# Kernel optimization log

Hardware: AMD Instinct MI355X
Metric: run time of the kernel (lower is better)

## Reference

```python
import jax, jax.numpy as jnp
import numpy as np

N = 50000
E = 800000
IN_DIM = 128
OUT_DIM = 128


def setup_inputs() -> dict:
    key = jax.random.key(0)
    k1, k2, k3, k4 = jax.random.split(key, 4)
    x = jax.random.normal(k1, (N, IN_DIM), dtype=jnp.float32)
    edge_index = jax.random.randint(k2, (2, E), 0, N, dtype=jnp.int64)
    # Linear(in_dim*2, out_dim) params
    W = jax.random.normal(k3, (2 * IN_DIM, OUT_DIM), dtype=jnp.float32) * (1.0 / np.sqrt(2 * IN_DIM))
    b = jax.random.normal(k4, (OUT_DIM,), dtype=jnp.float32) * 0.01
    return {"x": x, "edge_index": edge_index, "W": W, "b": b}


def reference(x, edge_index, W, b):
    src, dst = edge_index[0], edge_index[1]
    diff = x[src] - x[dst]                              # (E, C)
    # segment-max over destination nodes; empty segments get -inf identity
    seg_max = jax.ops.segment_max(diff, dst, num_segments=N)  # (N, C)
    counts = jax.ops.segment_sum(jnp.ones((E,), dtype=jnp.int32), dst, num_segments=N)
    # original code leaves zeros for nodes with no incoming edges
    max_diff = jnp.where((counts > 0)[:, None], seg_max, jnp.zeros_like(seg_max))
    x_cat = jnp.concatenate([x, max_diff], axis=-1)     # (N, 2C)
    return x_cat @ W + b
```

## Files before the change

### kernel.cpp

```cpp
#include <hip/hip_runtime.h>
#include <math.h>

#define NN 50000
#define NE 800000
#define CD 128
#define PB 3200
#define OVCAP 65536

typedef __attribute__((ext_vector_type(8))) short short8;
typedef __attribute__((ext_vector_type(4))) float f32x4;
typedef unsigned long long ull;


__device__ inline unsigned pack2bf(float lo, float hi) {
    unsigned a = __float_as_uint(lo), b = __float_as_uint(hi);
    a = (a + 0x7fffu + ((a >> 16) & 1u)) >> 16;
    b = (b + 0x7fffu + ((b >> 16) & 1u)) & 0xffff0000u;
    return a | b;
}

__device__ inline unsigned short f2bf(float f) {
    unsigned u = __float_as_uint(f);
    return (unsigned short)((u + 0x7fffu + ((u >> 16) & 1u)) >> 16);
}

__device__ inline void fmax8(float* m, uint4 v) {
    m[0] = fmaxf(m[0], __uint_as_float(v.x << 16));
    m[1] = fmaxf(m[1], __uint_as_float(v.x & 0xffff0000u));
    m[2] = fmaxf(m[2], __uint_as_float(v.y << 16));
    m[3] = fmaxf(m[3], __uint_as_float(v.y & 0xffff0000u));
    m[4] = fmaxf(m[4], __uint_as_float(v.z << 16));
    m[5] = fmaxf(m[5], __uint_as_float(v.z & 0xffff0000u));
    m[6] = fmaxf(m[6], __uint_as_float(v.w << 16));
    m[7] = fmaxf(m[7], __uint_as_float(v.w & 0xffff0000u));
}


__global__ __launch_bounds__(256) void prep_k(const int* __restrict__ ei,
                                              const float* __restrict__ x,
                                              const float* __restrict__ W,
                                              int* __restrict__ cnt,
                                              unsigned short* __restrict__ bkt,
                                              unsigned* __restrict__ ovl,
                                              unsigned* __restrict__ xb,
                                              unsigned short* __restrict__ wt) {
    int tid0 = blockIdx.x * 256 + threadIdx.x;
    int phase = blockIdx.x & 1;

    for (int p = 0; p < 2; p++) {
        if ((p ^ phase) == 0) {
            for (int e = tid0; e < NE; e += PB * 256) {
                int s = ei[e];
                int d = ei[NE + e];
                int k = atomicAdd(&cnt[d], 1);
                if (k < 64) {
                    bkt[(size_t)d * 64 + k] = (unsigned short)s;
                } else {
                    unsigned oi = atomicAdd((unsigned*)&cnt[NN], 1u);
                    if (oi < OVCAP) ovl[oi] = ((unsigned)d << 16) | (unsigned)s;
                }
            }
        } else {
            for (int i = tid0; i < NN * CD / 4; i += PB * 256) {
                float4 v = ((const float4*)x)[i];
                uint2 r;
                r.x = pack2bf(v.x, v.y);
                r.y = pack2bf(v.z, v.w);
                ((uint2*)xb)[i] = r;
            }
        }
    }
    for (int i = tid0; i < 2 * CD * CD; i += PB * 256) {
        int n = i >> 8, k = i & 255;
        wt[(size_t)n * 256 + k] = f2bf(W[(size_t)k * 128 + n]);
    }
}


__global__ __launch_bounds__(256) void fused_k(const unsigned* __restrict__ xb,
                                               const int* __restrict__ cnt,
                                               const unsigned short* __restrict__ bkt,
                                               const unsigned* __restrict__ ovl,
                                               const short* __restrict__ wt,
                                               const float* __restrict__ bias,
                                               float* __restrict__ out) {
    __shared__ unsigned short amx[32][136];

    int t = threadIdx.x;
    int nbase = blockIdx.x * 32;
    int w = t >> 6, lane = t & 63;
    int q = lane >> 4, c = lane & 15;

#pragma unroll 1
    for (int j = 0; j < 2; j++) {
        int ln = w * 8 + j * 4 + q;
        int node = nbase + ln;
        int cntv = (node < NN) ? cnt[node] : 0;
        int cn = min(cntv, 64);
        const unsigned short* brow = bkt + (size_t)node * 64;
        float m[8];
#pragma unroll
        for (int i = 0; i < 8; i++) m[i] = -INFINITY;

        for (int base = 0; base < cn; base += 8) {
            uint4 pk = *(const uint4*)(brow + base);
            int s0 = (int)(pk.x & 0xffffu), s1 = (int)(pk.x >> 16);
            int s2 = (int)(pk.y & 0xffffu), s3 = (int)(pk.y >> 16);
            int s4 = (int)(pk.z & 0xffffu), s5 = (int)(pk.z >> 16);
            int s6 = (int)(pk.w & 0xffffu), s7 = (int)(pk.w >> 16);
            if (base + 8 <= cn) {
                fmax8(m, *(const uint4*)(xb + (size_t)s0 * 64 + c * 4));
                fmax8(m, *(const uint4*)(xb + (size_t)s1 * 64 + c * 4));
                fmax8(m, *(const uint4*)(xb + (size_t)s2 * 64 + c * 4));
                fmax8(m, *(const uint4*)(xb + (size_t)s3 * 64 + c * 4));
                fmax8(m, *(const uint4*)(xb + (size_t)s4 * 64 + c * 4));
                fmax8(m, *(const uint4*)(xb + (size_t)s5 * 64 + c * 4));
                fmax8(m, *(const uint4*)(xb + (size_t)s6 * 64 + c * 4));
                fmax8(m, *(const uint4*)(xb + (size_t)s7 * 64 + c * 4));
            } else {
                if (base + 0 < cn) fmax8(m, *(const uint4*)(xb + (size_t)s0 * 64 + c * 4));
                if (base + 1 < cn) fmax8(m, *(const uint4*)(xb + (size_t)s1 * 64 + c * 4));
                if (base + 2 < cn) fmax8(m, *(const uint4*)(xb + (size_t)s2 * 64 + c * 4));
                if (base + 3 < cn) fmax8(m, *(const uint4*)(xb + (size_t)s3 * 64 + c * 4));
                if (base + 4 < cn) fmax8(m, *(const uint4*)(xb + (size_t)s4 * 64 + c * 4));
                if (base + 5 < cn) fmax8(m, *(const uint4*)(xb + (size_t)s5 * 64 + c * 4));
                if (base + 6 < cn) fmax8(m, *(const uint4*)(xb + (size_t)s6 * 64 + c * 4));
                if (base + 7 < cn) fmax8(m, *(const uint4*)(xb + (size_t)s7 * 64 + c * 4));
            }
        }
        if (cntv > 64) {
            unsigned no = (unsigned)cnt[NN];
            if (no > OVCAP) no = OVCAP;
            for (unsigned i2 = 0; i2 < no; i2++) {
                unsigned u = ovl[i2];
                if ((int)(u >> 16) == node)
                    fmax8(m, *(const uint4*)(xb + (size_t)(u & 0xffffu) * 64 + c * 4));
            }
        }
        uint4 r = make_uint4(0u, 0u, 0u, 0u);
        if (cntv > 0) {
            uint4 xd = *(const uint4*)(xb + (size_t)node * 64 + c * 4);
            float d0 = m[0] - __uint_as_float(xd.x << 16);
            float d1 = m[1] - __uint_as_float(xd.x & 0xffff0000u);
            float d2 = m[2] - __uint_as_float(xd.y << 16);
            float d3 = m[3] - __uint_as_float(xd.y & 0xffff0000u);
            float d4 = m[4] - __uint_as_float(xd.z << 16);
            float d5 = m[5] - __uint_as_float(xd.z & 0xffff0000u);
            float d6 = m[6] - __uint_as_float(xd.w << 16);
            float d7 = m[7] - __uint_as_float(xd.w & 0xffff0000u);
            r.x = pack2bf(d0, d1);
            r.y = pack2bf(d2, d3);
            r.z = pack2bf(d4, d5);
            r.w = pack2bf(d6, d7);
        }
        *(uint4*)&amx[ln][c * 8] = r;
    }
    __syncthreads();

    int mm = lane & 15, g = lane >> 4;
    int rt = w & 1, ch = w >> 1;
    int r0 = nbase + rt * 16;
    int row = r0 + mm;
    bool rowok = row < NN;

    f32x4 acc[4];
#pragma unroll
    for (int ct = 0; ct < 4; ct++) {
        float bv = bias[ch * 64 + ct * 16 + mm];
        acc[ct] = (f32x4){bv, bv, bv, bv};
    }

    const short* xbs = (const short*)xb;
#pragma unroll
    for (int kc = 0; kc < 8; kc++) {
        int k0 = kc * 32;
        short8 a;
        if (kc < 4) {
            a = (short8){0, 0, 0, 0, 0, 0, 0, 0};
            if (rowok) a = *(const short8*)(xbs + (size_t)row * 128 + k0 + g * 8);
        } else {
            a = *(const short8*)&amx[rt * 16 + mm][(k0 - 128) + g * 8];
        }
#pragma unroll
        for (int ct = 0; ct < 4; ct++) {
            short8 b = *(const short8*)(wt + (size_t)(ch * 64 + ct * 16 + mm) * 256 + k0 + g * 8);
            acc[ct] = __builtin_amdgcn_mfma_f32_16x16x32_bf16(a, b, acc[ct], 0, 0, 0);
        }
    }

#pragma unroll
    for (int ct = 0; ct < 4; ct++) {
#pragma unroll
        for (int i = 0; i < 4; i++) {
            int rr = r0 + g * 4 + i;
            if (rr < NN) out[(size_t)rr * 128 + ch * 64 + ct * 16 + mm] = acc[ct][i];
        }
    }
}


extern "C" void kernel_launch(void* const* d_in, const int* in_sizes, int n_in,
                              void* d_out, int out_size, void* d_ws, size_t ws_size,
                              hipStream_t stream) {
    const float* x = (const float*)d_in[0];
    const int* ei = (const int*)d_in[1];
    const float* W = (const float*)d_in[2];
    const float* bias = (const float*)d_in[3];
    float* out = (float*)d_out;

    int* wsi = (int*)d_ws;
    int* cnt = wsi;
    unsigned short* bkt = (unsigned short*)(wsi + 50016);
    unsigned* xb = (unsigned*)(wsi + 1650016);
    unsigned short* wt = (unsigned short*)(wsi + 4850016);
    unsigned* ovl = (unsigned*)(wsi + 4866400);

    hipMemsetAsync(cnt, 0, 50016 * sizeof(int), stream);

    prep_k<<<PB, 256, 0, stream>>>(ei, x, W, cnt, bkt, ovl, xb, wt);
    fused_k<<<(NN + 31) / 32, 256, 0, stream>>>(xb, cnt, bkt, ovl, (const short*)wt,
                                                bias, out);
}
```

Baseline: 190.8 us.

## Merge prep and fused kernels into one cooperative persistent kernel with grid sync

Combines the bucketing/conversion kernel and the gather-max-plus-MFMA kernel into a single cooperative launch, separated by a grid-wide barrier. The second phase becomes a persistent loop over node tiles. The aim is to remove one kernel launch and the gap between the two kernels. In exchange the grid size is capped by occupancy, the prep phase has fewer threads, a grid sync is added, and the cooperative launch has its own overhead.

```diff
diff --git a/kernel.cpp b/kernel.cpp
--- a/kernel.cpp
+++ b/kernel.cpp
@@ -1,10 +1,13 @@
 #include <hip/hip_runtime.h>
+#include <hip/hip_cooperative_groups.h>
 #include <math.h>
+
+namespace cg = cooperative_groups;
 
 #define NN 50000
 #define NE 800000
 #define CD 128
-#define PB 3200
+#define NTILE 1563
 #define OVCAP 65536
 
 typedef __attribute__((ext_vector_type(8))) short short8;
@@ -36,20 +39,26 @@
 }
 
 
-__global__ __launch_bounds__(256) void prep_k(const int* __restrict__ ei,
-                                              const float* __restrict__ x,
-                                              const float* __restrict__ W,
-                                              int* __restrict__ cnt,
-                                              unsigned short* __restrict__ bkt,
-                                              unsigned* __restrict__ ovl,
-                                              unsigned* __restrict__ xb,
-                                              unsigned short* __restrict__ wt) {
-    int tid0 = blockIdx.x * 256 + threadIdx.x;
+__global__ __launch_bounds__(256, 4) void mono_k(const int* __restrict__ ei,
+                                                 const float* __restrict__ x,
+                                                 const float* __restrict__ W,
+                                                 const float* __restrict__ bias,
+                                                 float* __restrict__ out,
+                                                 int* __restrict__ cnt,
+                                                 unsigned short* __restrict__ bkt,
+                                                 unsigned* __restrict__ ovl,
+                                                 unsigned* __restrict__ xb,
+                                                 unsigned short* __restrict__ wt) {
+    __shared__ unsigned short amx[32][136];
+
+    int t = threadIdx.x;
+    int tid0 = blockIdx.x * 256 + t;
+    int gsz = gridDim.x * 256;
     int phase = blockIdx.x & 1;
 
     for (int p = 0; p < 2; p++) {
         if ((p ^ phase) == 0) {
-            for (int e = tid0; e < NE; e += PB * 256) {
+            for (int e = tid0; e < NE; e += gsz) {
                 int s = ei[e];
                 int d = ei[NE + e];
                 int k = atomicAdd(&cnt[d], 1);
@@ -61,7 +70,7 @@
                 }
             }
         } else {
-            for (int i = tid0; i < NN * CD / 4; i += PB * 256) {
+            for (int i = tid0; i < NN * CD / 4; i += gsz) {
                 float4 v = ((const float4*)x)[i];
                 uint2 r;
                 r.x = pack2bf(v.x, v.y);
@@ -70,131 +79,125 @@
             }
         }
     }
-    for (int i = tid0; i < 2 * CD * CD; i += PB * 256) {
+    for (int i = tid0; i < 2 * CD * CD; i += gsz) {
         int n = i >> 8, k = i & 255;
         wt[(size_t)n * 256 + k] = f2bf(W[(size_t)k * 128 + n]);
     }
-}
-
-
-__global__ __launch_bounds__(256) void fused_k(const unsigned* __restrict__ xb,
-                                               const int* __restrict__ cnt,
-                                               const unsigned short* __restrict__ bkt,
-                                               const unsigned* __restrict__ ovl,
-                                               const short* __restrict__ wt,
-                                               const float* __restrict__ bias,
-                                               float* __restrict__ out) {
-    __shared__ unsigned short amx[32][136];
-
-    int t = threadIdx.x;
-    int nbase = blockIdx.x * 32;
+
+    cg::this_grid().sync();
+
     int w = t >> 6, lane = t & 63;
     int q = lane >> 4, c = lane & 15;
-
-#pragma unroll 1
-    for (int j = 0; j < 2; j++) {
-        int ln = w * 8 + j * 4 + q;
-        int node = nbase + ln;
-        int cntv = (node < NN) ? cnt[node] : 0;
-        int cn = min(cntv, 64);
-        const unsigned short* brow = bkt + (size_t)node * 64;
-        float m[8];
-#pragma unroll
-        for (int i = 0; i < 8; i++) m[i] = -INFINITY;
-
-        for (int base = 0; base < cn; base += 8) {
-            uint4 pk = *(const uint4*)(brow + base);
-            int s0 = (int)(pk.x & 0xffffu), s1 = (int)(pk.x >> 16);
-            int s2 = (int)(pk.y & 0xffffu), s3 = (int)(pk.y >> 16);
-            int s4 = (int)(pk.z & 0xffffu), s5 = (int)(pk.z >> 16);
-            int s6 = (int)(pk.w & 0xffffu), s7 = (int)(pk.w >> 16);
-            if (base + 8 <= cn) {
-                fmax8(m, *(const uint4*)(xb + (size_t)s0 * 64 + c * 4));
-                fmax8(m, *(const uint4*)(xb + (size_t)s1 * 64 + c * 4));
-                fmax8(m, *(const uint4*)(xb + (size_t)s2 * 64 + c * 4));
-                fmax8(m, *(const uint4*)(xb + (size_t)s3 * 64 + c * 4));
-                fmax8(m, *(const uint4*)(xb + (size_t)s4 * 64 + c * 4));
-                fmax8(m, *(const uint4*)(xb + (size_t)s5 * 64 + c * 4));
-                fmax8(m, *(const uint4*)(xb + (size_t)s6 * 64 + c * 4));
-                fmax8(m, *(const uint4*)(xb + (size_t)s7 * 64 + c * 4));
-            } else {
-                if (base + 0 < cn) fmax8(m, *(const uint4*)(xb + (size_t)s0 * 64 + c * 4));
-                if (base + 1 < cn) fmax8(m, *(const uint4*)(xb + (size_t)s1 * 64 + c * 4));
-                if (base + 2 < cn) fmax8(m, *(const uint4*)(xb + (size_t)s2 * 64 + c * 4));
-                if (base + 3 < cn) fmax8(m, *(const uint4*)(xb + (size_t)s3 * 64 + c * 4));
-                if (base + 4 < cn) fmax8(m, *(const uint4*)(xb + (size_t)s4 * 64 + c * 4));
-                if (base + 5 < cn) fmax8(m, *(const uint4*)(xb + (size_t)s5 * 64 + c * 4));
-                if (base + 6 < cn) fmax8(m, *(const uint4*)(xb + (size_t)s6 * 64 + c * 4));
-                if (base + 7 < cn) fmax8(m, *(const uint4*)(xb + (size_t)s7 * 64 + c * 4));
-            }
-        }
-        if (cntv > 64) {
-            unsigned no = (unsigned)cnt[NN];
-            if (no > OVCAP) no = OVCAP;
-            for (unsigned i2 = 0; i2 < no; i2++) {
-                unsigned u = ovl[i2];
-                if ((int)(u >> 16) == node)
-                    fmax8(m, *(const uint4*)(xb + (size_t)(u & 0xffffu) * 64 + c * 4));
-            }
-        }
-        uint4 r = make_uint4(0u, 0u, 0u, 0u);
-        if (cntv > 0) {
-            uint4 xd = *(const uint4*)(xb + (size_t)node * 64 + c * 4);
-            float d0 = m[0] - __uint_as_float(xd.x << 16);
-            float d1 = m[1] - __uint_as_float(xd.x & 0xffff0000u);
-            float d2 = m[2] - __uint_as_float(xd.y << 16);
-            float d3 = m[3] - __uint_as_float(xd.y & 0xffff0000u);
-            float d4 = m[4] - __uint_as_float(xd.z << 16);
-            float d5 = m[5] - __uint_as_float(xd.z & 0xffff0000u);
-            float d6 = m[6] - __uint_as_float(xd.w << 16);
-            float d7 = m[7] - __uint_as_float(xd.w & 0xffff0000u);
-            r.x = pack2bf(d0, d1);
-            r.y = pack2bf(d2, d3);
-            r.z = pack2bf(d4, d5);
-            r.w = pack2bf(d6, d7);
-        }
-        *(uint4*)&amx[ln][c * 8] = r;
-    }
-    __syncthreads();
-
     int mm = lane & 15, g = lane >> 4;
     int rt = w & 1, ch = w >> 1;
-    int r0 = nbase + rt * 16;
-    int row = r0 + mm;
-    bool rowok = row < NN;
-
-    f32x4 acc[4];
-#pragma unroll
-    for (int ct = 0; ct < 4; ct++) {
-        float bv = bias[ch * 64 + ct * 16 + mm];
-        acc[ct] = (f32x4){bv, bv, bv, bv};
-    }
-
-    const short* xbs = (const short*)xb;
-#pragma unroll
-    for (int kc = 0; kc < 8; kc++) {
-        int k0 = kc * 32;
-        short8 a;
-        if (kc < 4) {
-            a = (short8){0, 0, 0, 0, 0, 0, 0, 0};
-            if (rowok) a = *(const short8*)(xbs + (size_t)row * 128 + k0 + g * 8);
-        } else {
-            a = *(const short8*)&amx[rt * 16 + mm][(k0 - 128) + g * 8];
-        }
+
+    for (int tile = blockIdx.x; tile < NTILE; tile += gridDim.x) {
+        int nbase = tile * 32;
+
+#pragma unroll 1
+        for (int j = 0; j < 2; j++) {
+            int ln = w * 8 + j * 4 + q;
+            int node = nbase + ln;
+            int cntv = (node < NN) ? cnt[node] : 0;
+            int cn = min(cntv, 64);
+            const unsigned short* brow = bkt + (size_t)node * 64;
+            float m[8];
+#pragma unroll
+            for (int i = 0; i < 8; i++) m[i] = -INFINITY;
+
+            for (int base = 0; base < cn; base += 8) {
+                uint4 pk = *(const uint4*)(brow + base);
+                int s0 = (int)(pk.x & 0xffffu), s1 = (int)(pk.x >> 16);
+                int s2 = (int)(pk.y & 0xffffu), s3 = (int)(pk.y >> 16);
+                int s4 = (int)(pk.z & 0xffffu), s5 = (int)(pk.z >> 16);
+                int s6 = (int)(pk.w & 0xffffu), s7 = (int)(pk.w >> 16);
+                if (base + 8 <= cn) {
+                    fmax8(m, *(const uint4*)(xb + (size_t)s0 * 64 + c * 4));
+                    fmax8(m, *(const uint4*)(xb + (size_t)s1 * 64 + c * 4));
+                    fmax8(m, *(const uint4*)(xb + (size_t)s2 * 64 + c * 4));
+                    fmax8(m, *(const uint4*)(xb + (size_t)s3 * 64 + c * 4));
+                    fmax8(m, *(const uint4*)(xb + (size_t)s4 * 64 + c * 4));
+                    fmax8(m, *(const uint4*)(xb + (size_t)s5 * 64 + c * 4));
+                    fmax8(m, *(const uint4*)(xb + (size_t)s6 * 64 + c * 4));
+                    fmax8(m, *(const uint4*)(xb + (size_t)s7 * 64 + c * 4));
+                } else {
+                    if (base + 0 < cn) fmax8(m, *(const uint4*)(xb + (size_t)s0 * 64 + c * 4));
+                    if (base + 1 < cn) fmax8(m, *(const uint4*)(xb + (size_t)s1 * 64 + c * 4));
+                    if (base + 2 < cn) fmax8(m, *(const uint4*)(xb + (size_t)s2 * 64 + c * 4));
+                    if (base + 3 < cn) fmax8(m, *(const uint4*)(xb + (size_t)s3 * 64 + c * 4));
+                    if (base + 4 < cn) fmax8(m, *(const uint4*)(xb + (size_t)s4 * 64 + c * 4));
+                    if (base + 5 < cn) fmax8(m, *(const uint4*)(xb + (size_t)s5 * 64 + c * 4));
+                    if (base + 6 < cn) fmax8(m, *(const uint4*)(xb + (size_t)s6 * 64 + c * 4));
+                    if (base + 7 < cn) fmax8(m, *(const uint4*)(xb + (size_t)s7 * 64 + c * 4));
+                }
+            }
+            if (cntv > 64) {
+                unsigned no = (unsigned)cnt[NN];
+                if (no > OVCAP) no = OVCAP;
+                for (unsigned i2 = 0; i2 < no; i2++) {
+                    unsigned u = ovl[i2];
+                    if ((int)(u >> 16) == node)
+                        fmax8(m, *(const uint4*)(xb + (size_t)(u & 0xffffu) * 64 + c * 4));
+                }
+            }
+            uint4 r = make_uint4(0u, 0u, 0u, 0u);
+            if (cntv > 0) {
+                uint4 xd = *(const uint4*)(xb + (size_t)node * 64 + c * 4);
+                float d0 = m[0] - __uint_as_float(xd.x << 16);
+                float d1 = m[1] - __uint_as_float(xd.x & 0xffff0000u);
+                float d2 = m[2] - __uint_as_float(xd.y << 16);
+                float d3 = m[3] - __uint_as_float(xd.y & 0xffff0000u);
+                float d4 = m[4] - __uint_as_float(xd.z << 16);
+                float d5 = m[5] - __uint_as_float(xd.z & 0xffff0000u);
+                float d6 = m[6] - __uint_as_float(xd.w << 16);
+                float d7 = m[7] - __uint_as_float(xd.w & 0xffff0000u);
+                r.x = pack2bf(d0, d1);
+                r.y = pack2bf(d2, d3);
+                r.z = pack2bf(d4, d5);
+                r.w = pack2bf(d6, d7);
+            }
+            *(uint4*)&amx[ln][c * 8] = r;
+        }
+        __syncthreads();
+
+        int r0 = nbase + rt * 16;
+        int row = r0 + mm;
+        bool rowok = row < NN;
+
+        f32x4 acc[4];
 #pragma unroll
         for (int ct = 0; ct < 4; ct++) {
-            short8 b = *(const short8*)(wt + (size_t)(ch * 64 + ct * 16 + mm) * 256 + k0 + g * 8);
-            acc[ct] = __builtin_amdgcn_mfma_f32_16x16x32_bf16(a, b, acc[ct], 0, 0, 0);
-        }
-    }
-
-#pragma unroll
-    for (int ct = 0; ct < 4; ct++) {
-#pragma unroll
-        for (int i = 0; i < 4; i++) {
-            int rr = r0 + g * 4 + i;
-            if (rr < NN) out[(size_t)rr * 128 + ch * 64 + ct * 16 + mm] = acc[ct][i];
-        }
+            float bv = bias[ch * 64 + ct * 16 + mm];
+            acc[ct] = (f32x4){bv, bv, bv, bv};
+        }
+
+        const short* xbs = (const short*)xb;
+#pragma unroll
+        for (int kc = 0; kc < 8; kc++) {
+            int k0 = kc * 32;
+            short8 a;
+            if (kc < 4) {
+                a = (short8){0, 0, 0, 0, 0, 0, 0, 0};
+                if (rowok) a = *(const short8*)(xbs + (size_t)row * 128 + k0 + g * 8);
+            } else {
+                a = *(const short8*)&amx[rt * 16 + mm][(k0 - 128) + g * 8];
+            }
+#pragma unroll
+            for (int ct = 0; ct < 4; ct++) {
+                short8 b = *(const short8*)(wt + (size_t)(ch * 64 + ct * 16 + mm) * 256 + k0 + g * 8);
+                acc[ct] = __builtin_amdgcn_mfma_f32_16x16x32_bf16(a, b, acc[ct], 0, 0, 0);
+            }
+        }
+
+#pragma unroll
+        for (int ct = 0; ct < 4; ct++) {
+#pragma unroll
+            for (int i = 0; i < 4; i++) {
+                int rr = r0 + g * 4 + i;
+                if (rr < NN) out[(size_t)rr * 128 + ch * 64 + ct * 16 + mm] = acc[ct][i];
+            }
+        }
+        __syncthreads();
     }
 }
 
@@ -215,9 +218,20 @@
     unsigned short* wt = (unsigned short*)(wsi + 4850016);
     unsigned* ovl = (unsigned*)(wsi + 4866400);
 
+    static int gridBlocks = 0;
+    if (gridBlocks == 0) {
+        int perCU = 0, numCU = 0;
+        hipOccupancyMaxActiveBlocksPerMultiprocessor(&perCU, (const void*)mono_k, 256, 0);
+        hipDeviceGetAttribute(&numCU, hipDeviceAttributeMultiprocessorCount, 0);
+        long gb = (long)perCU * (long)numCU;
+        if (gb < 256) gb = 1024;
+        if (gb > 2048) gb = 2048;
+        gridBlocks = (int)gb;
+    }
+
     hipMemsetAsync(cnt, 0, 50016 * sizeof(int), stream);
 
-    prep_k<<<PB, 256, 0, stream>>>(ei, x, W, cnt, bkt, ovl, xb, wt);
-    fused_k<<<(NN + 31) / 32, 256, 0, stream>>>(xb, cnt, bkt, ovl, (const short*)wt,
-                                                bias, out);
-}
+    void* args[] = {(void*)&ei, (void*)&x, (void*)&W, (void*)&bias, (void*)&out,
+                    (void*)&cnt, (void*)&bkt, (void*)&ovl, (void*)&xb, (void*)&wt};
+    hipLaunchCooperativeKernel((void*)mono_k, dim3(gridBlocks), dim3(256), args, 0, stream);
+}
```

Measured after the change: 336.3 us. +76.3%, slower.

## Split fused gather+GEMM kernel into separate gather and MFMA GEMM kernels

Applied to the files above, without the earlier changes.

The fused kernel is replaced by two kernels. A 128-thread gather kernel computes each node's bf16 segment-max difference, one node per 16-lane group, and writes it into the unused second half of each output row. A GEMM kernel then loads its A fragments for both the x half and the max-diff half into registers, synchronizes, and writes fp32 results over the same rows. The goal is more memory-level parallelism and better load balance in the irregular gather, with no shared-memory staging. The cost is an extra launch and an extra global write and read of the max-diff tile, plus reliance on an in-place read-before-write ordering inside each GEMM block.

```diff
diff --git a/kernel.cpp b/kernel.cpp
--- a/kernel.cpp
+++ b/kernel.cpp
@@ -9,7 +9,6 @@
 
 typedef __attribute__((ext_vector_type(8))) short short8;
 typedef __attribute__((ext_vector_type(4))) float f32x4;
-typedef unsigned long long ull;
 
 
 __device__ inline unsigned pack2bf(float lo, float hi) {
@@ -77,92 +76,103 @@
 }
 
 
-__global__ __launch_bounds__(256) void fused_k(const unsigned* __restrict__ xb,
-                                               const int* __restrict__ cnt,
-                                               const unsigned short* __restrict__ bkt,
-                                               const unsigned* __restrict__ ovl,
-                                               const short* __restrict__ wt,
-                                               const float* __restrict__ bias,
-                                               float* __restrict__ out) {
-    __shared__ unsigned short amx[32][136];
-
+__global__ __launch_bounds__(128) void gather_k(const unsigned* __restrict__ xb,
+                                                const int* __restrict__ cnt,
+                                                const unsigned short* __restrict__ bkt,
+                                                const unsigned* __restrict__ ovl,
+                                                unsigned* __restrict__ outu) {
     int t = threadIdx.x;
-    int nbase = blockIdx.x * 32;
+    int q = t >> 4, c = t & 15;
+    int node = blockIdx.x * 8 + q;
+    int cntv = cnt[node];
+    int cn = min(cntv, 64);
+    const unsigned short* brow = bkt + (size_t)node * 64;
+
+    float m[8];
+#pragma unroll
+    for (int i = 0; i < 8; i++) m[i] = -INFINITY;
+
+    for (int base = 0; base < cn; base += 8) {
+        uint4 pk = *(const uint4*)(brow + base);
+        int s0 = (int)(pk.x & 0xffffu), s1 = (int)(pk.x >> 16);
+        int s2 = (int)(pk.y & 0xffffu), s3 = (int)(pk.y >> 16);
+        int s4 = (int)(pk.z & 0xffffu), s5 = (int)(pk.z >> 16);
+        int s6 = (int)(pk.w & 0xffffu), s7 = (int)(pk.w >> 16);
+        if (base + 8 <= cn) {
+            fmax8(m, *(const uint4*)(xb + (size_t)s0 * 64 + c * 4));
+            fmax8(m, *(const uint4*)(xb + (size_t)s1 * 64 + c * 4));
+            fmax8(m, *(const uint4*)(xb + (size_t)s2 * 64 + c * 4));
+            fmax8(m, *(const uint4*)(xb + (size_t)s3 * 64 + c * 4));
+            fmax8(m, *(const uint4*)(xb + (size_t)s4 * 64 + c * 4));
+            fmax8(m, *(const uint4*)(xb + (size_t)s5 * 64 + c * 4));
+            fmax8(m, *(const uint4*)(xb + (size_t)s6 * 64 + c * 4));
+            fmax8(m, *(const uint4*)(xb + (size_t)s7 * 64 + c * 4));
+        } else {
+            if (base + 0 < cn) fmax8(m, *(const uint4*)(xb + (size_t)s0 * 64 + c * 4));
+            if (base + 1 < cn) fmax8(m, *(const uint4*)(xb + (size_t)s1 * 64 + c * 4));
+            if (base + 2 < cn) fmax8(m, *(const uint4*)(xb + (size_t)s2 * 64 + c * 4));
+            if (base + 3 < cn) fmax8(m, *(const uint4*)(xb + (size_t)s3 * 64 + c * 4));
+            if (base + 4 < cn) fmax8(m, *(const uint4*)(xb + (size_t)s4 * 64 + c * 4));
+            if (base + 5 < cn) fmax8(m, *(const uint4*)(xb + (size_t)s5 * 64 + c * 4));
+            if (base + 6 < cn) fmax8(m, *(const uint4*)(xb + (size_t)s6 * 64 + c * 4));
+            if (base + 7 < cn) fmax8(m, *(const uint4*)(xb + (size_t)s7 * 64 + c * 4));
+        }
+    }
+    if (cntv > 64) {
+        unsigned no = (unsigned)cnt[NN];
+        if (no > OVCAP) no = OVCAP;
+        for (unsigned i2 = 0; i2 < no; i2++) {
+            unsigned u = ovl[i2];
+            if ((int)(u >> 16) == node)
+                fmax8(m, *(const uint4*)(xb + (size_t)(u & 0xffffu) * 64 + c * 4));
+        }
+    }
+    uint4 r = make_uint4(0u, 0u, 0u, 0u);
+    if (cntv > 0) {
+        uint4 xd = *(const uint4*)(xb + (size_t)node * 64 + c * 4);
+        float d0 = m[0] - __uint_as_float(xd.x << 16);
+        float d1 = m[1] - __uint_as_float(xd.x & 0xffff0000u);
+        float d2 = m[2] - __uint_as_float(xd.y << 16);
+        float d3 = m[3] - __uint_as_float(xd.y & 0xffff0000u);
+        float d4 = m[4] - __uint_as_float(xd.z << 16);
+        float d5 = m[5] - __uint_as_float(xd.z & 0xffff0000u);
+        float d6 = m[6] - __uint_as_float(xd.w << 16);
+        float d7 = m[7] - __uint_as_float(xd.w & 0xffff0000u);
+        r.x = pack2bf(d0, d1);
+        r.y = pack2bf(d2, d3);
+        r.z = pack2bf(d4, d5);
+        r.w = pack2bf(d6, d7);
+    }
+    *(uint4*)(outu + (size_t)node * 128 + 64 + c * 4) = r;
+}
+
+
+__global__ __launch_bounds__(256) void gemm_k(const unsigned* __restrict__ xb,
+                                              const unsigned* __restrict__ amxu,
+                                              const short* __restrict__ wt,
+                                              const float* __restrict__ bias,
+                                              float* __restrict__ out) {
+    int t = threadIdx.x;
     int w = t >> 6, lane = t & 63;
-    int q = lane >> 4, c = lane & 15;
-
-#pragma unroll 1
-    for (int j = 0; j < 2; j++) {
-        int ln = w * 8 + j * 4 + q;
-        int node = nbase + ln;
-        int cntv = (node < NN) ? cnt[node] : 0;
-        int cn = min(cntv, 64);
-        const unsigned short* brow = bkt + (size_t)node * 64;
-        float m[8];
-#pragma unroll
-        for (int i = 0; i < 8; i++) m[i] = -INFINITY;
-
-        for (int base = 0; base < cn; base += 8) {
-            uint4 pk = *(const uint4*)(brow + base);
-            int s0 = (int)(pk.x & 0xffffu), s1 = (int)(pk.x >> 16);
-            int s2 = (int)(pk.y & 0xffffu), s3 = (int)(pk.y >> 16);
-            int s4 = (int)(pk.z & 0xffffu), s5 = (int)(pk.z >> 16);
-            int s6 = (int)(pk.w & 0xffffu), s7 = (int)(pk.w >> 16);
-            if (base + 8 <= cn) {
-                fmax8(m, *(const uint4*)(xb + (size_t)s0 * 64 + c * 4));
-                fmax8(m, *(const uint4*)(xb + (size_t)s1 * 64 + c * 4));
-                fmax8(m, *(const uint4*)(xb + (size_t)s2 * 64 + c * 4));
-                fmax8(m, *(const uint4*)(xb + (size_t)s3 * 64 + c * 4));
-                fmax8(m, *(const uint4*)(xb + (size_t)s4 * 64 + c * 4));
-                fmax8(m, *(const uint4*)(xb + (size_t)s5 * 64 + c * 4));
-                fmax8(m, *(const uint4*)(xb + (size_t)s6 * 64 + c * 4));
-                fmax8(m, *(const uint4*)(xb + (size_t)s7 * 64 + c * 4));
-            } else {
-                if (base + 0 < cn) fmax8(m, *(const uint4*)(xb + (size_t)s0 * 64 + c * 4));
-                if (base + 1 < cn) fmax8(m, *(const uint4*)(xb + (size_t)s1 * 64 + c * 4));
-                if (base + 2 < cn) fmax8(m, *(const uint4*)(xb + (size_t)s2 * 64 + c * 4));
-                if (base + 3 < cn) fmax8(m, *(const uint4*)(xb + (size_t)s3 * 64 + c * 4));
-                if (base + 4 < cn) fmax8(m, *(const uint4*)(xb + (size_t)s4 * 64 + c * 4));
-                if (base + 5 < cn) fmax8(m, *(const uint4*)(xb + (size_t)s5 * 64 + c * 4));
-                if (base + 6 < cn) fmax8(m, *(const uint4*)(xb + (size_t)s6 * 64 + c * 4));
-                if (base + 7 < cn) fmax8(m, *(const uint4*)(xb + (size_t)s7 * 64 + c * 4));
-            }
-        }
-        if (cntv > 64) {
-            unsigned no = (unsigned)cnt[NN];
-            if (no > OVCAP) no = OVCAP;
-            for (unsigned i2 = 0; i2 < no; i2++) {
-                unsigned u = ovl[i2];
-                if ((int)(u >> 16) == node)
-                    fmax8(m, *(const uint4*)(xb + (size_t)(u & 0xffffu) * 64 + c * 4));
-            }
-        }
-        uint4 r = make_uint4(0u, 0u, 0u, 0u);
-        if (cntv > 0) {
-            uint4 xd = *(const uint4*)(xb + (size_t)node * 64 + c * 4);
-            float d0 = m[0] - __uint_as_float(xd.x << 16);
-            float d1 = m[1] - __uint_as_float(xd.x & 0xffff0000u);
-            float d2 = m[2] - __uint_as_float(xd.y << 16);
-            float d3 = m[3] - __uint_as_float(xd.y & 0xffff0000u);
-            float d4 = m[4] - __uint_as_float(xd.z << 16);
-            float d5 = m[5] - __uint_as_float(xd.z & 0xffff0000u);
-            float d6 = m[6] - __uint_as_float(xd.w << 16);
-            float d7 = m[7] - __uint_as_float(xd.w & 0xffff0000u);
-            r.x = pack2bf(d0, d1);
-            r.y = pack2bf(d2, d3);
-            r.z = pack2bf(d4, d5);
-            r.w = pack2bf(d6, d7);
-        }
-        *(uint4*)&amx[ln][c * 8] = r;
-    }
-    __syncthreads();
-
     int mm = lane & 15, g = lane >> 4;
     int rt = w & 1, ch = w >> 1;
+    int nbase = blockIdx.x * 32;
     int r0 = nbase + rt * 16;
     int row = r0 + mm;
     bool rowok = row < NN;
 
+    uint4 afr[8];
+#pragma unroll
+    for (int kc = 0; kc < 4; kc++)
+        afr[kc] = rowok ? *(const uint4*)(xb + (size_t)row * 64 + kc * 16 + g * 4)
+                        : make_uint4(0u, 0u, 0u, 0u);
+#pragma unroll
+    for (int kc = 4; kc < 8; kc++)
+        afr[kc] = rowok ? *(const uint4*)(amxu + (size_t)row * 128 + 64 + (kc - 4) * 16 + g * 4)
+                        : make_uint4(0u, 0u, 0u, 0u);
+
+    __syncthreads();
+
     f32x4 acc[4];
 #pragma unroll
     for (int ct = 0; ct < 4; ct++) {
@@ -170,20 +180,13 @@
         acc[ct] = (f32x4){bv, bv, bv, bv};
     }
 
-    const short* xbs = (const short*)xb;
 #pragma unroll
     for (int kc = 0; kc < 8; kc++) {
-        int k0 = kc * 32;
         short8 a;
-        if (kc < 4) {
-            a = (short8){0, 0, 0, 0, 0, 0, 0, 0};
-            if (rowok) a = *(const short8*)(xbs + (size_t)row * 128 + k0 + g * 8);
-        } else {
-            a = *(const short8*)&amx[rt * 16 + mm][(k0 - 128) + g * 8];
-        }
+        __builtin_memcpy(&a, &afr[kc], 16);
 #pragma unroll
         for (int ct = 0; ct < 4; ct++) {
-            short8 b = *(const short8*)(wt + (size_t)(ch * 64 + ct * 16 + mm) * 256 + k0 + g * 8);
+            short8 b = *(const short8*)(wt + (size_t)(ch * 64 + ct * 16 + mm) * 256 + kc * 32 + g * 8);
             acc[ct] = __builtin_amdgcn_mfma_f32_16x16x32_bf16(a, b, acc[ct], 0, 0, 0);
         }
     }
@@ -218,6 +221,7 @@
     hipMemsetAsync(cnt, 0, 50016 * sizeof(int), stream);
 
     prep_k<<<PB, 256, 0, stream>>>(ei, x, W, cnt, bkt, ovl, xb, wt);
-    fused_k<<<(NN + 31) / 32, 256, 0, stream>>>(xb, cnt, bkt, ovl, (const short*)wt,
-                                                bias, out);
-}
+    gather_k<<<NN / 8, 128, 0, stream>>>(xb, cnt, bkt, ovl, (unsigned*)out);
+    gemm_k<<<(NN + 31) / 32, 256, 0, stream>>>(xb, (const unsigned*)out, (const short*)wt,
+                                               bias, out);
+}
```

Result: no change. 189.5 us (-0.7%).
